# Kernel optimization log

Hardware: AMD Instinct MI355X
Metric: run time of the kernel (lower is better)

Reference implementation:

```python
import jax, jax.numpy as jnp
import numpy as np

B, N, D = 32, 50000, 64  # batch, node_num, num_inputs


def setup_inputs() -> dict:
    key = jax.random.key(0)
    k1, k2, k3 = jax.random.split(key, 3)
    x = jax.random.normal(k1, (B, N, D), dtype=jnp.float32)
    # xavier_uniform_ with gain=1.414 on a (2D, 1) matrix: bound = gain*sqrt(6/(fan_in+fan_out))
    bound = 1.414 * np.sqrt(6.0 / (2 * D + 1))
    a = jax.random.uniform(k2, (2 * D, 1), minval=-bound, maxval=bound, dtype=jnp.float32)
    adj_mask = jax.random.randint(k3, (N,), 0, 2).astype(jnp.int32)
    node_index = 123  # scalar target-node index
    return {"x": x, "a": a, "node_index": node_index, "adj_mask": adj_mask}


def reference(x, a, node_index, adj_mask):
    # torch: concat([x[:, idx].expand(node_num), x], -1) @ a  ==  x[:, idx] @ a[:D] + x @ a[D:]
    d = x.shape[-1]
    a_tgt = a[:d, 0]   # weights applied to the (broadcast) target-node features
    a_src = a[d:, 0]   # weights applied to every node's own features
    tgt_score = x[:, node_index] @ a_tgt          # [B]
    e = jax.nn.leaky_relu(tgt_score[:, None] + x @ a_src, negative_slope=0.01)  # [B, N]
    neg = jnp.asarray(-9e15, e.dtype)
    masked = jnp.where(adj_mask > 0, e, neg)
    attention = jax.nn.softmax(masked, axis=1) * adj_mask.astype(e.dtype)[None, :]
    return attention
```

## Files before the change

### kernel.cpp

```cpp
#include <hip/hip_runtime.h>

#define NN 50000
#define DD 64
#define BB 32
#define TILE 256
#define NPB ((NN + TILE - 1) / TILE)

__global__ __launch_bounds__(256) void attn_pass1(
    const float* __restrict__ x, const float* __restrict__ a,
    const int* __restrict__ node_index, const int* __restrict__ adj,
    float* __restrict__ out, float* __restrict__ pbs )
{
    const int tid = threadIdx.x;
    const int b = blockIdx.y;
    const int rowBase = blockIdx.x * TILE;
    const int node = *node_index;

    __shared__ int   sh_adj[TILE];
    __shared__ float sh_p[TILE];
    __shared__ float sh_tgt;
    __shared__ float sh_part[4];

    {
        const int r = rowBase + tid;
        sh_adj[tid] = (r < NN) ? adj[r] : 0;
    }

    if (tid < 64) {
        float v = x[(size_t)b * NN * DD + (size_t)node * DD + tid] * a[tid];
        #pragma unroll
        for (int o = 32; o >= 1; o >>= 1) v += __shfl_xor(v, o, 64);
        if (tid == 0) sh_tgt = v;
    }
    __syncthreads();
    const float tgt = sh_tgt;

    const int wave = tid >> 6;
    const int lane = tid & 63;
    const int c  = lane & 3;
    const int rg = lane >> 2;

    const float4* a4 = (const float4*)(a + DD);
    const float4 av0 = a4[c + 0];
    const float4 av1 = a4[c + 4];
    const float4 av2 = a4[c + 8];
    const float4 av3 = a4[c + 12];

    const float* xb = x + (size_t)b * NN * DD;
    float local = 0.f;

    #pragma unroll
    for (int i = 0; i < 4; i++) {
        const int lrow = wave * 64 + i * 16 + rg;
        const int msk = sh_adj[lrow];
        float s = 0.f;
        if (msk > 0) {
            const float4* xr = (const float4*)(xb + (size_t)(rowBase + lrow) * DD);
            const float4 v0 = xr[c + 0];
            const float4 v1 = xr[c + 4];
            const float4 v2 = xr[c + 8];
            const float4 v3 = xr[c + 12];
            s  = v0.x * av0.x + v0.y * av0.y + v0.z * av0.z + v0.w * av0.w;
            s += v1.x * av1.x + v1.y * av1.y + v1.z * av1.z + v1.w * av1.w;
            s += v2.x * av2.x + v2.y * av2.y + v2.z * av2.z + v2.w * av2.w;
            s += v3.x * av3.x + v3.y * av3.y + v3.z * av3.z + v3.w * av3.w;
        }
        s += __shfl_xor(s, 1, 64);
        s += __shfl_xor(s, 2, 64);
        if (c == 0) {
            float p = 0.f;
            if (msk > 0) {
                const float z = tgt + s;
                const float e = (z > 0.f) ? z : 0.01f * z;
                p = __expf(e);
            }
            sh_p[lrow] = p;
            local += p;
        }
    }

    #pragma unroll
    for (int o = 32; o >= 1; o >>= 1) local += __shfl_xor(local, o, 64);
    if (lane == 0) sh_part[wave] = local;
    __syncthreads();
    if (tid == 0)
        pbs[b * NPB + blockIdx.x] = sh_part[0] + sh_part[1] + sh_part[2] + sh_part[3];

    {
        const int r = rowBase + tid;
        if (r < NN) out[(size_t)b * NN + r] = sh_p[tid];
    }
}

__global__ __launch_bounds__(256) void attn_pass2(
    float* __restrict__ out, const float* __restrict__ pbs)
{
    const int tid = threadIdx.x;
    const int b = blockIdx.y;
    __shared__ float sh[4];

    float v = (tid < NPB) ? pbs[b * NPB + tid] : 0.f;
    #pragma unroll
    for (int o = 32; o >= 1; o >>= 1) v += __shfl_xor(v, o, 64);
    if ((tid & 63) == 0) sh[tid >> 6] = v;
    __syncthreads();
    const float inv = 1.0f / (sh[0] + sh[1] + sh[2] + sh[3]);

    const int N4 = NN / 4;
    const int f = blockIdx.x * blockDim.x + tid;
    if (f < N4) {
        float4* p = (float4*)out + (size_t)b * N4 + f;
        float4 w = *p;
        w.x *= inv; w.y *= inv; w.z *= inv; w.w *= inv;
        *p = w;
    }
}

extern "C" void kernel_launch(void* const* d_in, const int* in_sizes, int n_in,
                              void* d_out, int out_size, void* d_ws, size_t ws_size,
                              hipStream_t stream) {
    const float* x = (const float*)d_in[0];
    const float* a = (const float*)d_in[1];
    const int* node_index = (const int*)d_in[2];
    const int* adj = (const int*)d_in[3];
    float* out = (float*)d_out;
    float* pbs = (float*)d_ws;

    dim3 g1(NPB, BB);
    attn_pass1<<<g1, 256, 0, stream>>>(x, a, node_index, adj, out, pbs);

    dim3 g2((NN / 4 + 255) / 256, BB);
    attn_pass2<<<g2, 256, 0, stream>>>(out, pbs);
}
```

Measured before the change: 492.8 us.

## Assign one thread per row for full 64-wide dot product in pass1

Pass1 changes from four lanes cooperating on each row, with shuffle reductions and shared-memory staging, to one thread computing a whole row's 64-element dot product. The a vector is held in registers, the mask is read straight from global memory, and output is written directly, so the shared arrays and per-row shuffles go away. The cost is uncoalesced memory access: each lane reads a 256-byte row with a large stride between lanes, and register pressure rises from 16 float4 loads plus 64 weights per thread.

```diff
diff --git a/kernel.cpp b/kernel.cpp
--- a/kernel.cpp
+++ b/kernel.cpp
@@ -13,18 +13,14 @@
 {
     const int tid = threadIdx.x;
     const int b = blockIdx.y;
-    const int rowBase = blockIdx.x * TILE;
+    const int r = blockIdx.x * TILE + tid;
     const int node = *node_index;
 
-    __shared__ int   sh_adj[TILE];
-    __shared__ float sh_p[TILE];
     __shared__ float sh_tgt;
-    __shared__ float sh_part[4];
+    __shared__ float sh_red[4];
 
-    {
-        const int r = rowBase + tid;
-        sh_adj[tid] = (r < NN) ? adj[r] : 0;
-    }
+    int msk = 0;
+    if (r < NN) msk = adj[r];
 
     if (tid < 64) {
         float v = x[(size_t)b * NN * DD + (size_t)node * DD + tid] * a[tid];
@@ -32,64 +28,42 @@
         for (int o = 32; o >= 1; o >>= 1) v += __shfl_xor(v, o, 64);
         if (tid == 0) sh_tgt = v;
     }
+
+    float av[DD];
+    #pragma unroll
+    for (int j = 0; j < DD; j++) av[j] = a[DD + j];
+
     __syncthreads();
     const float tgt = sh_tgt;
 
-    const int wave = tid >> 6;
-    const int lane = tid & 63;
-    const int c  = lane & 3;
-    const int rg = lane >> 2;
+    float p = 0.f;
+    if (msk > 0) {
+        const float4* __restrict__ xr =
+            (const float4*)(x + (size_t)b * NN * DD + (size_t)r * DD);
+        float4 v[16];
+        #pragma unroll
+        for (int k = 0; k < 16; k++) v[k] = xr[k];
+        float s0 = 0.f, s1 = 0.f, s2 = 0.f, s3 = 0.f;
+        #pragma unroll
+        for (int k = 0; k < 16; k++) {
+            s0 += v[k].x * av[4 * k + 0];
+            s1 += v[k].y * av[4 * k + 1];
+            s2 += v[k].z * av[4 * k + 2];
+            s3 += v[k].w * av[4 * k + 3];
+        }
+        const float z = tgt + ((s0 + s1) + (s2 + s3));
+        const float e = (z > 0.f) ? z : 0.01f * z;
+        p = __expf(e);
+    }
+    if (r < NN) out[(size_t)b * NN + r] = p;
 
-    const float4* a4 = (const float4*)(a + DD);
-    const float4 av0 = a4[c + 0];
-    const float4 av1 = a4[c + 4];
-    const float4 av2 = a4[c + 8];
-    const float4 av3 = a4[c + 12];
-
-    const float* xb = x + (size_t)b * NN * DD;
-    float local = 0.f;
-
+    float loc = p;
     #pragma unroll
-    for (int i = 0; i < 4; i++) {
-        const int lrow = wave * 64 + i * 16 + rg;
-        const int msk = sh_adj[lrow];
-        float s = 0.f;
-        if (msk > 0) {
-            const float4* xr = (const float4*)(xb + (size_t)(rowBase + lrow) * DD);
-            const float4 v0 = xr[c + 0];
-            const float4 v1 = xr[c + 4];
-            const float4 v2 = xr[c + 8];
-            const float4 v3 = xr[c + 12];
-            s  = v0.x * av0.x + v0.y * av0.y + v0.z * av0.z + v0.w * av0.w;
-            s += v1.x * av1.x + v1.y * av1.y + v1.z * av1.z + v1.w * av1.w;
-            s += v2.x * av2.x + v2.y * av2.y + v2.z * av2.z + v2.w * av2.w;
-            s += v3.x * av3.x + v3.y * av3.y + v3.z * av3.z + v3.w * av3.w;
-        }
-        s += __shfl_xor(s, 1, 64);
-        s += __shfl_xor(s, 2, 64);
-        if (c == 0) {
-            float p = 0.f;
-            if (msk > 0) {
-                const float z = tgt + s;
-                const float e = (z > 0.f) ? z : 0.01f * z;
-                p = __expf(e);
-            }
-            sh_p[lrow] = p;
-            local += p;
-        }
-    }
-
-    #pragma unroll
-    for (int o = 32; o >= 1; o >>= 1) local += __shfl_xor(local, o, 64);
-    if (lane == 0) sh_part[wave] = local;
+    for (int o = 32; o >= 1; o >>= 1) loc += __shfl_xor(loc, o, 64);
+    if ((tid & 63) == 0) sh_red[tid >> 6] = loc;
     __syncthreads();
     if (tid == 0)
-        pbs[b * NPB + blockIdx.x] = sh_part[0] + sh_part[1] + sh_part[2] + sh_part[3];
-
-    {
-        const int r = rowBase + tid;
-        if (r < NN) out[(size_t)b * NN + r] = sh_p[tid];
-    }
+        pbs[b * NPB + blockIdx.x] = sh_red[0] + sh_red[1] + sh_red[2] + sh_red[3];
 }
 
 __global__ __launch_bounds__(256) void attn_pass2(
```

After: 495.4 us. About the same (+0.5%).
